# Optimization experiments

Measured on AMD Instinct MI355X. Metric: run time of the kernel, lower is better.

The kernel has to match this reference:

```python
import jax, jax.numpy as jnp
import numpy as np

WIN = (7, 7)          # window_size (M, M)
DIM = 128             # C
HEADS = 4
B = 64                # images
NW = 64               # windows per image
NG = WIN[0] * WIN[1]  # 49 tokens per window
NT = 3136             # total patches per image (56x56)


def _relative_position_index(wh, ww):
    # Faithful to the TF code (default 'xy' meshgrid ordering, global token at (0,0))
    coords = np.stack(np.meshgrid(np.arange(wh), np.arange(ww)))        # (2, ww, wh)
    flat = coords.reshape(2, wh * ww)                                    # (2, M^2)
    flat1 = np.concatenate([flat, np.array([[0], [0]])], axis=1)         # (2, M^2+1)
    rel = flat[:, :, None] - flat1[:, None, :]                           # (2, M^2, M^2+1)
    rel = rel.transpose(1, 2, 0).astype(np.int32)
    rel[:, :, 0] += wh - 1
    rel[:, :, 1] += ww - 1
    rel[:, :, 0] *= 2 * ww - 1
    return rel.sum(-1)                                                   # (M^2, M^2+1)


def setup_inputs() -> dict:
    key = jax.random.key(0)
    ks = jax.random.split(key, 9)
    C, H = DIM, HEADS
    B_ = B * NW
    table_sz = (2 * WIN[0] - 1) * (2 * WIN[1] - 1)  # 169
    return {
        "x": jax.random.normal(ks[0], (B_, NG, C), jnp.float32),
        "xtotal": jax.random.normal(ks[1], (B, NT, C), jnp.float32),
        "xavg": jax.random.normal(ks[2], (B, 1, C), jnp.float32),
        "mask": jnp.zeros((NW, NG, NG + 1), jnp.float32),
        "W_q": jax.random.normal(ks[3], (C, C), jnp.float32) * (C ** -0.5),
        "b_q": jax.random.normal(ks[4], (C,), jnp.float32) * 0.02,
        "W_kv": jax.random.normal(ks[5], (C, 2 * C), jnp.float32) * (C ** -0.5),
        "b_kv": jax.random.normal(ks[6], (2 * C,), jnp.float32) * 0.02,
        "bias_table": jax.random.normal(ks[7], (table_sz, H), jnp.float32) * 0.02,
        "rel_idx": jnp.asarray(_relative_position_index(*WIN), jnp.int32),
    }


def reference(x, xtotal, xavg, mask, W_q, b_q, W_kv, b_kv, bias_table, rel_idx):
    B_, NGl, C = x.shape
    Bl = xavg.shape[0]
    H = bias_table.shape[1]
    d = C // H
    scale = d ** -0.5
    N = NGl + 1

    # window path: concat repeated global token, project kv / q
    xavgR = jnp.repeat(xavg, B_ // Bl, axis=0)               # (B_, 1, C)
    x_c = jnp.concatenate([x, xavgR], axis=1)                # (B_, N, C)
    kv = (x_c @ W_kv + b_kv).reshape(B_, N, 2, H, d).transpose(2, 0, 3, 1, 4)
    k, v = kv[0], kv[1]                                      # (B_, H, N, d)
    q = ((x @ W_q + b_q).reshape(B_, NGl, H, d).transpose(0, 2, 1, 3)) * scale

    attn = jnp.einsum('bhnd,bhmd->bhnm', q, k)               # (B_, H, NG, N)
    bias = bias_table[rel_idx.reshape(-1)].reshape(NGl, N, H).transpose(2, 0, 1)
    attn = attn + bias[None]
    nW = mask.shape[0]
    attn = attn.reshape(B_ // nW, nW, H, NGl, N) + mask[None, :, None]
    attn = jax.nn.softmax(attn.reshape(B_, H, NGl, N), axis=-1)
    x_out = jnp.einsum('bhnm,bhmd->bhnd', attn, v).transpose(0, 2, 1, 3).reshape(B_, NGl, C)

    # global path: q_avg (NOT scaled in the original), attends over all patches
    Nt = xtotal.shape[1]
    kvg = (xtotal @ W_kv + b_kv).reshape(Bl, Nt, 2, H, d).transpose(2, 0, 3, 1, 4)
    kg, vg = kvg[0], kvg[1]                                  # (B, H, Nt, d)
    q_avg = (xavg @ W_q + b_q).reshape(Bl, 1, H, d).transpose(0, 2, 1, 3)
    attng = jax.nn.softmax(jnp.einsum('bhqd,bhmd->bhqm', q_avg, kg), axis=-1)
    xavg_out = jnp.einsum('bhqm,bhmd->bhqd', attng, vg).transpose(0, 2, 1, 3).reshape(Bl, 1, C)
    return x_out, xavg_out
```

## Files before the change

### kernel.cpp

```cpp
#include <hip/hip_runtime.h>
#include <hip/hip_bf16.h>

#define NB_  4096
#define NG_  49
#define NC_  128
#define NH_  4
#define DH_  32
#define NN_  50
#define NIMG 64
#define NT_  3136
#define NCHK 8
#define CROWS 392
#define SCALE_ 0.17677669529663687f

#define WT_LO_OFF 49152
#define BM_OFF    98304
#define FBASE  573440
#define U_F    (FBASE)
#define CST_F  (FBASE + 32768)
#define WACC_F (FBASE + 33024)
#define SUM_F  (FBASE + 65792)
#define CNT_F  (FBASE + 66048)

typedef unsigned short u16;
typedef unsigned int   u32;
typedef __attribute__((ext_vector_type(8))) short bf16x8;
typedef __attribute__((ext_vector_type(4))) float f32x4;

__device__ __forceinline__ float b2f(u16 u) {
    union { u32 i; float f; } v; v.i = ((u32)u) << 16; return v.f;
}
__device__ __forceinline__ u16 f2b(float f) {
    union { float f; u32 i; } v; v.f = f;
    u32 x = v.i;
    return (u16)((x + 0x7fffu + ((x >> 16) & 1u)) >> 16);
}
__device__ __forceinline__ u32 pk2(float a, float b) {
    union { __hip_bfloat162 h2; u32 u; } v;
    v.h2 = __float22bfloat162_rn(make_float2(a, b));
    return v.u;
}

extern "C" __global__ __launch_bounds__(256)
void prep_kernel(const float* __restrict__ Wq, const float* __restrict__ Wkv,
                 const float* __restrict__ btab, const int* __restrict__ ridx,
                 const float* __restrict__ mask, const float* __restrict__ xavg,
                 const float* __restrict__ bq, const float* __restrict__ bkv,
                 u16* __restrict__ ws)
{
    __shared__ int   ridxS[NG_ * NN_];
    __shared__ float btabS[169 * NH_];
    __shared__ float xavgS[NC_];
    __shared__ float qaS[NC_];
    const int t = threadIdx.x, b = blockIdx.x;
    if (b < 24) {
        const int fp  = b * 4 + (t >> 6);
        const int lane = t & 63, l15 = lane & 15, g = lane >> 4;
        const int kt = fp & 3, rest = fp >> 2, jt = rest & 1, hty = rest >> 1;
        const int ty = hty % 3, hh = hty / 3;
        const int jc = 32 * hh + 16 * jt + l15;
        const float* src; int stride; float qs = 1.f;
        if (ty == 0)      { src = Wq  + jc;       stride = NC_;     qs = SCALE_; }
        else if (ty == 1) { src = Wkv + jc;       stride = 2 * NC_; }
        else              { src = Wkv + NC_ + jc; stride = 2 * NC_; }
        const int c0 = 32 * kt + 8 * g;
        u32 hi[4], lo[4];
        #pragma unroll
        for (int p = 0; p < 4; ++p) {
            const int c = c0 + 2 * p;
            float w0 = src[(size_t)c * stride] * qs;
            float w1 = src[(size_t)(c + 1) * stride] * qs;
            u16 h0 = f2b(w0), h1 = f2b(w1);
            hi[p] = (u32)h0 | ((u32)h1 << 16);
            lo[p] = (u32)f2b(w0 - b2f(h0)) | ((u32)f2b(w1 - b2f(h1)) << 16);
        }
        const size_t fo = ((size_t)fp * 64 + lane) * 8;
        *(uint4*)(ws + fo)             = make_uint4(hi[0], hi[1], hi[2], hi[3]);
        *(uint4*)(ws + WT_LO_OFF + fo) = make_uint4(lo[0], lo[1], lo[2], lo[3]);
    } else if (b < 88) {
        const int wx = b - 24;
        for (int i = t; i < NG_ * NN_; i += 256) ridxS[i] = ridx[i];
        for (int i = t; i < 169 * NH_; i += 256) btabS[i] = btab[i];
        __syncthreads();
        for (int i = t; i < NH_ * 16 * 64; i += 256) {
            const int lane = i & 63, tile = (i >> 6) & 15, h = i >> 10;
            const int n  = 16 * (tile >> 2) + (lane & 15);
            const int m0 = 16 * (tile & 3) + 4 * (lane >> 4);
            u16 vv[4];
            #pragma unroll
            for (int e = 0; e < 4; ++e) {
                const int m = m0 + e;
                float val = -1e30f;
                if (n < NG_ && m < NN_)
                    val = btabS[ridxS[n * NN_ + m] * NH_ + h] + mask[((size_t)wx * NG_ + n) * NN_ + m];
                vv[e] = f2b(val);
            }
            u32* dst = (u32*)(ws + BM_OFF + ((size_t)((wx * NH_ + h) * 16 + tile) * 64 + lane) * 4);
            dst[0] = (u32)vv[0] | ((u32)vv[1] << 16);
            dst[1] = (u32)vv[2] | ((u32)vv[3] << 16);
        }
    } else {
        const int img = b - 88;
        float* wsF = (float*)ws;
        if (t < NC_) xavgS[t] = xavg[img * NC_ + t];
        __syncthreads();
        if (t < NC_) {
            float acc = bq[t];
            for (int c = 0; c < NC_; ++c) acc += xavgS[c] * Wq[c * NC_ + t];
            qaS[t] = acc;
        }
        __syncthreads();
        if (t < NC_) {
            const int c = t;
            const float* wr = Wkv + (size_t)c * 256;
            #pragma unroll
            for (int h = 0; h < NH_; ++h) {
                float acc = 0.f;
                #pragma unroll
                for (int j = 0; j < 32; ++j) acc += wr[h * 32 + j] * qaS[h * 32 + j];
                wsF[U_F + img * 512 + h * 128 + c] = acc;
            }
            #pragma unroll
            for (int h = 0; h < NH_; ++h) wsF[WACC_F + img * 512 + h * 128 + t] = 0.f;
        } else if (t < NC_ + NH_) {
            const int h = t - NC_;
            float acc = 0.f;
            for (int j = 0; j < 32; ++j) acc += qaS[h * 32 + j] * bkv[h * 32 + j];
            wsF[CST_F + img * 4 + h] = acc;
            wsF[SUM_F + img * 4 + h] = 0.f;
        } else if (t == NC_ + NH_) {
            ((int*)wsF)[CNT_F + img] = 0;
        }
    }
}

struct ChunkShared {
    float waccS[4][4][128];
    float esumS[4][4];
    float sumS[4];
    int   flagS;
};

extern "C" __global__ __launch_bounds__(256, 3)
void wa2_kernel(const float* __restrict__ x, const float* __restrict__ xtotal,
                const float* __restrict__ xavg,
                const float* __restrict__ Wq, const float* __restrict__ bq,
                const float* __restrict__ Wkv, const float* __restrict__ bkv,
                float* __restrict__ out, u16* __restrict__ ws)
{
    __shared__ ChunkShared smc;
    const int t = threadIdx.x;
    const int blk = blockIdx.x;
    const int lane = t & 63, wv = t >> 6;

    if (blk >= NIMG * NCHK) {
        const int wb   = blk - NIMG * NCHK;
        const int img  = wb >> 6;
        const int widx = wb & 63;
        const int h = wv, l15 = lane & 15, g = lane >> 4;

        bf16x8 xf[4][4];
        {
            const float* xbase = x + (size_t)wb * (NG_ * NC_);
            #pragma unroll
            for (int rt = 0; rt < 4; ++rt) {
                const int row = 16 * rt + l15;
                const float* rp = (row < NG_) ? (xbase + (size_t)row * NC_)
                                              : (xavg + (size_t)img * NC_);
                const bool vld = (row <= NG_);
                #pragma unroll
                for (int kt = 0; kt < 4; ++kt) {
                    float4 u0 = *(const float4*)(rp + 32 * kt + 8 * g);
                    float4 u1 = *(const float4*)(rp + 32 * kt + 8 * g + 4);
                    if (!vld) { u0 = make_float4(0.f,0.f,0.f,0.f); u1 = make_float4(0.f,0.f,0.f,0.f); }
                    union { u32 w[4]; bf16x8 v; } F;
                    F.w[0] = pk2(u0.x, u0.y); F.w[1] = pk2(u0.z, u0.w);
                    F.w[2] = pk2(u1.x, u1.y); F.w[3] = pk2(u1.z, u1.w);
                    xf[rt][kt] = F.v;
                }
            }
        }

        bf16x8 qf[4], kf[4];
        #pragma unroll
        for (int ty = 0; ty < 2; ++ty) {
            f32x4 acc[2][4];
            #pragma unroll
            for (int jt = 0; jt < 2; ++jt) {
                f32x4 cin;
                #pragma unroll
                for (int r = 0; r < 4; ++r) {
                    const int j = 32 * h + 16 * jt + 4 * g + r;
                    cin[r] = (ty == 0) ? bq[j] * SCALE_ : bkv[j];
                }
                #pragma unroll
                for (int rt = 0; rt < 4; ++rt) acc[jt][rt] = cin;
            }
            #pragma unroll
            for (int kt = 0; kt < 4; ++kt) {
                const int fpb = ((h * 3 + ty) * 2) * 4 + kt;
                const bf16x8 wh0 = *(const bf16x8*)(ws + ((size_t)fpb * 64 + lane) * 8);
                const bf16x8 wl0 = *(const bf16x8*)(ws + WT_LO_OFF + ((size_t)fpb * 64 + lane) * 8);
                const bf16x8 wh1 = *(const bf16x8*)(ws + ((size_t)(fpb + 4) * 64 + lane) * 8);
                const bf16x8 wl1 = *(const bf16x8*)(ws + WT_LO_OFF + ((size_t)(fpb + 4) * 64 + lane) * 8);
                #pragma unroll
                for (int rt = 0; rt < 4; ++rt) {
                    acc[0][rt] = __builtin_amdgcn_mfma_f32_16x16x32_bf16(wh0, xf[rt][kt], acc[0][rt], 0, 0, 0);
                    acc[0][rt] = __builtin_amdgcn_mfma_f32_16x16x32_bf16(wl0, xf[rt][kt], acc[0][rt], 0, 0, 0);
                    acc[1][rt] = __builtin_amdgcn_mfma_f32_16x16x32_bf16(wh1, xf[rt][kt], acc[1][rt], 0, 0, 0);
                    acc[1][rt] = __builtin_amdgcn_mfma_f32_16x16x32_bf16(wl1, xf[rt][kt], acc[1][rt], 0, 0, 0);
                }
            }
            #pragma unroll
            for (int rt = 0; rt < 4; ++rt) {
                union { u32 w[4]; bf16x8 v; } F;
                F.w[0] = pk2(acc[0][rt][0], acc[0][rt][1]);
                F.w[1] = pk2(acc[0][rt][2], acc[0][rt][3]);
                F.w[2] = pk2(acc[1][rt][0], acc[1][rt][1]);
                F.w[3] = pk2(acc[1][rt][2], acc[1][rt][3]);
                if (ty == 0) qf[rt] = F.v; else kf[rt] = F.v;
            }
        }

        bf16x8 vbf[2][2];
        {
            f32x4 vacc[4][2];
            #pragma unroll
            for (int tn = 0; tn < 2; ++tn) {
                const float bv = bkv[NC_ + 32 * h + 16 * tn + l15];
                #pragma unroll
                for (int tm = 0; tm < 4; ++tm) vacc[tm][tn] = (f32x4){bv, bv, bv, bv};
            }
            #pragma unroll
            for (int kt = 0; kt < 4; ++kt) {
                const int fpb = ((h * 3 + 2) * 2) * 4 + kt;
                const bf16x8 wh0 = *(const bf16x8*)(ws + ((size_t)fpb * 64 + lane) * 8);
                const bf16x8 wl0 = *(const bf16x8*)(ws + WT_LO_OFF + ((size_t)fpb * 64 + lane) * 8);
                const bf16x8 wh1 = *(const bf16x8*)(ws + ((size_t)(fpb + 4) * 64 + lane) * 8);
                const bf16x8 wl1 = *(const bf16x8*)(ws + WT_LO_OFF + ((size_t)(fpb + 4) * 64 + lane) * 8);
                #pragma unroll
                for (int tm = 0; tm < 4; ++tm) {
                    vacc[tm][0] = __builtin_amdgcn_mfma_f32_16x16x32_bf16(xf[tm][kt], wh0, vacc[tm][0], 0, 0, 0);
                    vacc[tm][0] = __builtin_amdgcn_mfma_f32_16x16x32_bf16(xf[tm][kt], wl0, vacc[tm][0], 0, 0, 0);
                    vacc[tm][1] = __builtin_amdgcn_mfma_f32_16x16x32_bf16(xf[tm][kt], wh1, vacc[tm][1], 0, 0, 0);
                    vacc[tm][1] = __builtin_amdgcn_mfma_f32_16x16x32_bf16(xf[tm][kt], wl1, vacc[tm][1], 0, 0, 0);
                }
            }
            #pragma unroll
            for (int kt2 = 0; kt2 < 2; ++kt2)
                #pragma unroll
                for (int tn = 0; tn < 2; ++tn) {
                    union { u32 w[4]; bf16x8 v; } F;
                    F.w[0] = pk2(vacc[2 * kt2][tn][0], vacc[2 * kt2][tn][1]);
                    F.w[1] = pk2(vacc[2 * kt2][tn][2], vacc[2 * kt2][tn][3]);
                    F.w[2] = pk2(vacc[2 * kt2 + 1][tn][0], vacc[2 * kt2 + 1][tn][1]);
                    F.w[3] = pk2(vacc[2 * kt2 + 1][tn][2], vacc[2 * kt2 + 1][tn][3]);
                    vbf[kt2][tn] = F.v;
                }
        }

        const u16* bmb = ws + BM_OFF + (size_t)(widx * NH_ + h) * 4096;
        #pragma unroll
        for (int tq = 0; tq < 4; ++tq) {
            f32x4 s[4];
            #pragma unroll
            for (int tk = 0; tk < 4; ++tk) {
                uint2 bm = *(const uint2*)(bmb + ((size_t)(tq * 4 + tk) * 64 + lane) * 4);
                f32x4 c0;
                c0[0] = b2f((u16)bm.x); c0[1] = b2f((u16)(bm.x >> 16));
                c0[2] = b2f((u16)bm.y); c0[3] = b2f((u16)(bm.y >> 16));
                s[tk] = __builtin_amdgcn_mfma_f32_16x16x32_bf16(kf[tk], qf[tq], c0, 0, 0, 0);
            }
            float mx = s[0][0];
            #pragma unroll
            for (int tk = 0; tk < 4; ++tk)
                #pragma unroll
                for (int r = 0; r < 4; ++r) mx = fmaxf(mx, s[tk][r]);
            mx = fmaxf(mx, __shfl_xor(mx, 16));
            mx = fmaxf(mx, __shfl_xor(mx, 32));
            float sum = 0.f;
            #pragma unroll
            for (int tk = 0; tk < 4; ++tk)
                #pragma unroll
                for (int r = 0; r < 4; ++r) {
                    float e = __expf(s[tk][r] - mx);
                    s[tk][r] = e;
                    sum += e;
                }
            sum += __shfl_xor(sum, 16);
            sum += __shfl_xor(sum, 32);
            const float inv = 1.f / sum;

            bf16x8 pa[2];
            #pragma unroll
            for (int kt2 = 0; kt2 < 2; ++kt2) {
                union { u32 w[4]; bf16x8 v; } P;
                P.w[0] = pk2(s[2 * kt2][0] * inv, s[2 * kt2][1] * inv);
                P.w[1] = pk2(s[2 * kt2][2] * inv, s[2 * kt2][3] * inv);
                P.w[2] = pk2(s[2 * kt2 + 1][0] * inv, s[2 * kt2 + 1][1] * inv);
                P.w[3] = pk2(s[2 * kt2 + 1][2] * inv, s[2 * kt2 + 1][3] * inv);
                pa[kt2] = P.v;
            }
            #pragma unroll
            for (int tn = 0; tn < 2; ++tn) {
                f32x4 o = {0.f, 0.f, 0.f, 0.f};
                o = __builtin_amdgcn_mfma_f32_16x16x32_bf16(pa[0], vbf[0][tn], o, 0, 0, 0);
                o = __builtin_amdgcn_mfma_f32_16x16x32_bf16(pa[1], vbf[1][tn], o, 0, 0, 0);
                #pragma unroll
                for (int r = 0; r < 4; ++r) {
                    const int row = 16 * tq + 4 * g + r;
                    if (row < NG_)
                        out[(size_t)wb * (NG_ * NC_) + (size_t)row * NC_ + 32 * h + 16 * tn + l15] = o[r];
                }
            }
        }
    } else {
        ChunkShared& S = smc;
        float* wsF = (float*)ws;
        const int img = blk >> 3, ch = blk & 7;
        const int c0 = (lane & 31) * 4, roff = lane >> 5;

        float4 uR[NH_]; float cstR[NH_];
        #pragma unroll
        for (int h = 0; h < NH_; ++h) {
            uR[h]  = *(const float4*)&wsF[U_F + img * 512 + h * 128 + c0];
            cstR[h] = wsF[CST_F + img * 4 + h];
        }

        float wacc[NH_][4] = {};
        float esum[NH_] = {0.f, 0.f, 0.f, 0.f};
        const float* xb = xtotal + ((size_t)img * NT_ + ch * CROWS) * NC_;
        for (int it = 0; it < CROWS / 8; ++it) {
            const int m = it * 8 + wv * 2 + roff;
            float4 xv = *(const float4*)&xb[(size_t)m * NC_ + c0];
            float s[NH_];
            #pragma unroll
            for (int h = 0; h < NH_; ++h)
                s[h] = xv.x * uR[h].x + xv.y * uR[h].y + xv.z * uR[h].z + xv.w * uR[h].w;
            #pragma unroll
            for (int off = 1; off < 32; off <<= 1) {
                #pragma unroll
                for (int h = 0; h < NH_; ++h) s[h] += __shfl_xor(s[h], off);
            }
            #pragma unroll
            for (int h = 0; h < NH_; ++h) {
                const float e = __expf(s[h] + cstR[h]);
                wacc[h][0] += e * xv.x; wacc[h][1] += e * xv.y;
                wacc[h][2] += e * xv.z; wacc[h][3] += e * xv.w;
                if ((lane & 31) == 0) esum[h] += e;
            }
        }

        #pragma unroll
        for (int h = 0; h < NH_; ++h) {
            #pragma unroll
            for (int i = 0; i < 4; ++i) wacc[h][i] += __shfl_xor(wacc[h][i], 32);
            esum[h] += __shfl_xor(esum[h], 32);
        }
        if (lane < 32) {
            #pragma unroll
            for (int h = 0; h < NH_; ++h)
                #pragma unroll
                for (int i = 0; i < 4; ++i) S.waccS[wv][h][c0 + i] = wacc[h][i];
            if (lane == 0) {
                #pragma unroll
                for (int h = 0; h < NH_; ++h) S.esumS[wv][h] = esum[h];
            }
        }
        __syncthreads();
        if (t < NC_) {
            #pragma unroll
            for (int h = 0; h < NH_; ++h) {
                float v = S.waccS[0][h][t] + S.waccS[1][h][t] + S.waccS[2][h][t] + S.waccS[3][h][t];
                atomicAdd(&wsF[WACC_F + img * 512 + h * 128 + t], v);
            }
        } else if (t < NC_ + NH_) {
            const int h = t - NC_;
            atomicAdd(&wsF[SUM_F + img * 4 + h],
                      S.esumS[0][h] + S.esumS[1][h] + S.esumS[2][h] + S.esumS[3][h]);
        }
        __threadfence();
        __syncthreads();
        if (t == 0) S.flagS = atomicAdd(&((int*)wsF)[CNT_F + img], 1);
        __syncthreads();
        if (S.flagS == NCHK - 1) {
            float* wS = &S.waccS[0][0][0];
            for (int i = t; i < 512; i += 256)
                wS[i] = atomicAdd(&wsF[WACC_F + img * 512 + i], 0.f);
            if (t < NH_) S.sumS[t] = atomicAdd(&wsF[SUM_F + img * 4 + t], 0.f);
            __syncthreads();
            if (t < NC_) {
                const int h = t >> 5;
                const float inv = 1.f / S.sumS[h];
                float acc = bkv[NC_ + t];
                for (int c = 0; c < NC_; ++c)
                    acc += (wS[h * 128 + c] * inv) * Wkv[(size_t)c * 256 + NC_ + t];
                out[(size_t)NB_ * (NG_ * NC_) + img * NC_ + t] = acc;
            }
        }
    }
}

extern "C" void kernel_launch(void* const* d_in, const int* in_sizes, int n_in,
                              void* d_out, int out_size, void* d_ws, size_t ws_size,
                              hipStream_t stream) {
    const float* x      = (const float*)d_in[0];
    const float* xtotal = (const float*)d_in[1];
    const float* xavg   = (const float*)d_in[2];
    const float* mask   = (const float*)d_in[3];
    const float* Wq     = (const float*)d_in[4];
    const float* bq     = (const float*)d_in[5];
    const float* Wkv    = (const float*)d_in[6];
    const float* bkv    = (const float*)d_in[7];
    const float* btab   = (const float*)d_in[8];
    const int*   ridx   = (const int*)d_in[9];
    float* outp = (float*)d_out;
    u16*   ws   = (u16*)d_ws;
    (void)in_sizes; (void)n_in; (void)out_size; (void)ws_size;

    prep_kernel<<<152, 256, 0, stream>>>(Wq, Wkv, btab, ridx, mask, xavg, bq, bkv, ws);
    wa2_kernel<<<NIMG * NCHK + NB_, 256, 0, stream>>>(x, xtotal, xavg, Wq, bq,
                                                      Wkv, bkv, outp, ws);
}
```

Baseline: 426.6 us.

## Stream x fragments per k-step, interleave weight hi/lo, raise occupancy, drop softmax max

Result: slower. 552.7 us (+29.6%).

```diff
diff --git a/kernel.cpp b/kernel.cpp
--- a/kernel.cpp
+++ b/kernel.cpp
@@ -13,7 +13,6 @@
 #define CROWS 392
 #define SCALE_ 0.17677669529663687f
 
-#define WT_LO_OFF 49152
 #define BM_OFF    98304
 #define FBASE  573440
 #define U_F    (FBASE)
@@ -39,6 +38,26 @@
     union { __hip_bfloat162 h2; u32 u; } v;
     v.h2 = __float22bfloat162_rn(make_float2(a, b));
     return v.u;
+}
+
+__device__ __forceinline__ void load_xf(const float* __restrict__ xbase,
+                                        const float* __restrict__ xavgp,
+                                        int kt, int l15, int g, bf16x8* xf)
+{
+    #pragma unroll
+    for (int rt = 0; rt < 4; ++rt) {
+        const int row = 16 * rt + l15;
+        const float* rp = (row < NG_) ? (xbase + (size_t)row * NC_) : xavgp;
+        const bool vld = (row <= NG_);
+        float4 u0 = *(const float4*)(rp + 32 * kt + 8 * g);
+        float4 u1 = *(const float4*)(rp + 32 * kt + 8 * g + 4);
+        union { u32 w[4]; bf16x8 v; } F;
+        F.w[0] = vld ? pk2(u0.x, u0.y) : 0u;
+        F.w[1] = vld ? pk2(u0.z, u0.w) : 0u;
+        F.w[2] = vld ? pk2(u1.x, u1.y) : 0u;
+        F.w[3] = vld ? pk2(u1.z, u1.w) : 0u;
+        xf[rt] = F.v;
+    }
 }
 
 extern "C" __global__ __launch_bounds__(256)
@@ -74,9 +93,9 @@
             hi[p] = (u32)h0 | ((u32)h1 << 16);
             lo[p] = (u32)f2b(w0 - b2f(h0)) | ((u32)f2b(w1 - b2f(h1)) << 16);
         }
-        const size_t fo = ((size_t)fp * 64 + lane) * 8;
-        *(uint4*)(ws + fo)             = make_uint4(hi[0], hi[1], hi[2], hi[3]);
-        *(uint4*)(ws + WT_LO_OFF + fo) = make_uint4(lo[0], lo[1], lo[2], lo[3]);
+        const size_t fo = ((size_t)fp * 64 + lane) * 16;
+        *(uint4*)(ws + fo)     = make_uint4(hi[0], hi[1], hi[2], hi[3]);
+        *(uint4*)(ws + fo + 8) = make_uint4(lo[0], lo[1], lo[2], lo[3]);
     } else if (b < 88) {
         const int wx = b - 24;
         for (int i = t; i < NG_ * NN_; i += 256) ridxS[i] = ridx[i];
@@ -141,7 +160,7 @@
     int   flagS;
 };
 
-extern "C" __global__ __launch_bounds__(256, 3)
+extern "C" __global__ __launch_bounds__(256, 4)
 void wa2_kernel(const float* __restrict__ x, const float* __restrict__ xtotal,
                 const float* __restrict__ xavg,
                 const float* __restrict__ Wq, const float* __restrict__ bq,
@@ -158,92 +177,89 @@
         const int img  = wb >> 6;
         const int widx = wb & 63;
         const int h = wv, l15 = lane & 15, g = lane >> 4;
-
-        bf16x8 xf[4][4];
+        const float* xbase = x + (size_t)wb * (NG_ * NC_);
+        const float* xavgp = xavg + (size_t)img * NC_;
+
+        bf16x8 qf[4], kf[4];
         {
-            const float* xbase = x + (size_t)wb * (NG_ * NC_);
-            #pragma unroll
-            for (int rt = 0; rt < 4; ++rt) {
-                const int row = 16 * rt + l15;
-                const float* rp = (row < NG_) ? (xbase + (size_t)row * NC_)
-                                              : (xavg + (size_t)img * NC_);
-                const bool vld = (row <= NG_);
-                #pragma unroll
-                for (int kt = 0; kt < 4; ++kt) {
-                    float4 u0 = *(const float4*)(rp + 32 * kt + 8 * g);
-                    float4 u1 = *(const float4*)(rp + 32 * kt + 8 * g + 4);
-                    if (!vld) { u0 = make_float4(0.f,0.f,0.f,0.f); u1 = make_float4(0.f,0.f,0.f,0.f); }
-                    union { u32 w[4]; bf16x8 v; } F;
-                    F.w[0] = pk2(u0.x, u0.y); F.w[1] = pk2(u0.z, u0.w);
-                    F.w[2] = pk2(u1.x, u1.y); F.w[3] = pk2(u1.z, u1.w);
-                    xf[rt][kt] = F.v;
-                }
-            }
-        }
-
-        bf16x8 qf[4], kf[4];
-        #pragma unroll
-        for (int ty = 0; ty < 2; ++ty) {
-            f32x4 acc[2][4];
+            f32x4 aq[2][4], ak[2][4];
             #pragma unroll
             for (int jt = 0; jt < 2; ++jt) {
-                f32x4 cin;
+                f32x4 cq, ck;
                 #pragma unroll
                 for (int r = 0; r < 4; ++r) {
                     const int j = 32 * h + 16 * jt + 4 * g + r;
-                    cin[r] = (ty == 0) ? bq[j] * SCALE_ : bkv[j];
-                }
-                #pragma unroll
-                for (int rt = 0; rt < 4; ++rt) acc[jt][rt] = cin;
+                    cq[r] = bq[j] * SCALE_;
+                    ck[r] = bkv[j];
+                }
+                #pragma unroll
+                for (int rt = 0; rt < 4; ++rt) { aq[jt][rt] = cq; ak[jt][rt] = ck; }
             }
             #pragma unroll
             for (int kt = 0; kt < 4; ++kt) {
-                const int fpb = ((h * 3 + ty) * 2) * 4 + kt;
-                const bf16x8 wh0 = *(const bf16x8*)(ws + ((size_t)fpb * 64 + lane) * 8);
-                const bf16x8 wl0 = *(const bf16x8*)(ws + WT_LO_OFF + ((size_t)fpb * 64 + lane) * 8);
-                const bf16x8 wh1 = *(const bf16x8*)(ws + ((size_t)(fpb + 4) * 64 + lane) * 8);
-                const bf16x8 wl1 = *(const bf16x8*)(ws + WT_LO_OFF + ((size_t)(fpb + 4) * 64 + lane) * 8);
+                bf16x8 xf[4];
+                load_xf(xbase, xavgp, kt, l15, g, xf);
+                const u16* wq0 = ws + ((size_t)((h * 3 + 0) * 8 + kt) * 64 + lane) * 16;
+                const u16* wk0 = ws + ((size_t)((h * 3 + 1) * 8 + kt) * 64 + lane) * 16;
+                const bf16x8 qh0 = *(const bf16x8*)(wq0);
+                const bf16x8 ql0 = *(const bf16x8*)(wq0 + 8);
+                const bf16x8 qh1 = *(const bf16x8*)(wq0 + 64 * 64);
+                const bf16x8 ql1 = *(const bf16x8*)(wq0 + 64 * 64 + 8);
+                const bf16x8 kh0 = *(const bf16x8*)(wk0);
+                const bf16x8 kl0 = *(const bf16x8*)(wk0 + 8);
+                const bf16x8 kh1 = *(const bf16x8*)(wk0 + 64 * 64);
+                const bf16x8 kl1 = *(const bf16x8*)(wk0 + 64 * 64 + 8);
                 #pragma unroll
                 for (int rt = 0; rt < 4; ++rt) {
-                    acc[0][rt] = __builtin_amdgcn_mfma_f32_16x16x32_bf16(wh0, xf[rt][kt], acc[0][rt], 0, 0, 0);
-                    acc[0][rt] = __builtin_amdgcn_mfma_f32_16x16x32_bf16(wl0, xf[rt][kt], acc[0][rt], 0, 0, 0);
-                    acc[1][rt] = __builtin_amdgcn_mfma_f32_16x16x32_bf16(wh1, xf[rt][kt], acc[1][rt], 0, 0, 0);
-                    acc[1][rt] = __builtin_amdgcn_mfma_f32_16x16x32_bf16(wl1, xf[rt][kt], acc[1][rt], 0, 0, 0);
+                    aq[0][rt] = __builtin_amdgcn_mfma_f32_16x16x32_bf16(qh0, xf[rt], aq[0][rt], 0, 0, 0);
+                    aq[0][rt] = __builtin_amdgcn_mfma_f32_16x16x32_bf16(ql0, xf[rt], aq[0][rt], 0, 0, 0);
+                    aq[1][rt] = __builtin_amdgcn_mfma_f32_16x16x32_bf16(qh1, xf[rt], aq[1][rt], 0, 0, 0);
+                    aq[1][rt] = __builtin_amdgcn_mfma_f32_16x16x32_bf16(ql1, xf[rt], aq[1][rt], 0, 0, 0);
+                    ak[0][rt] = __builtin_amdgcn_mfma_f32_16x16x32_bf16(kh0, xf[rt], ak[0][rt], 0, 0, 0);
+                    ak[0][rt] = __builtin_amdgcn_mfma_f32_16x16x32_bf16(kl0, xf[rt], ak[0][rt], 0, 0, 0);
+                    ak[1][rt] = __builtin_amdgcn_mfma_f32_16x16x32_bf16(kh1, xf[rt], ak[1][rt], 0, 0, 0);
+                    ak[1][rt] = __builtin_amdgcn_mfma_f32_16x16x32_bf16(kl1, xf[rt], ak[1][rt], 0, 0, 0);
                 }
             }
             #pragma unroll
             for (int rt = 0; rt < 4; ++rt) {
-                union { u32 w[4]; bf16x8 v; } F;
-                F.w[0] = pk2(acc[0][rt][0], acc[0][rt][1]);
-                F.w[1] = pk2(acc[0][rt][2], acc[0][rt][3]);
-                F.w[2] = pk2(acc[1][rt][0], acc[1][rt][1]);
-                F.w[3] = pk2(acc[1][rt][2], acc[1][rt][3]);
-                if (ty == 0) qf[rt] = F.v; else kf[rt] = F.v;
+                union { u32 w[4]; bf16x8 v; } FQ, FK;
+                FQ.w[0] = pk2(aq[0][rt][0], aq[0][rt][1]);
+                FQ.w[1] = pk2(aq[0][rt][2], aq[0][rt][3]);
+                FQ.w[2] = pk2(aq[1][rt][0], aq[1][rt][1]);
+                FQ.w[3] = pk2(aq[1][rt][2], aq[1][rt][3]);
+                FK.w[0] = pk2(ak[0][rt][0], ak[0][rt][1]);
+                FK.w[1] = pk2(ak[0][rt][2], ak[0][rt][3]);
+                FK.w[2] = pk2(ak[1][rt][0], ak[1][rt][1]);
+                FK.w[3] = pk2(ak[1][rt][2], ak[1][rt][3]);
+                qf[rt] = FQ.v; kf[rt] = FK.v;
             }
         }
 
         bf16x8 vbf[2][2];
         {
-            f32x4 vacc[4][2];
+            f32x4 av[4][2];
             #pragma unroll
             for (int tn = 0; tn < 2; ++tn) {
                 const float bv = bkv[NC_ + 32 * h + 16 * tn + l15];
                 #pragma unroll
-                for (int tm = 0; tm < 4; ++tm) vacc[tm][tn] = (f32x4){bv, bv, bv, bv};
+                for (int tm = 0; tm < 4; ++tm) av[tm][tn] = (f32x4){bv, bv, bv, bv};
             }
             #pragma unroll
             for (int kt = 0; kt < 4; ++kt) {
-                const int fpb = ((h * 3 + 2) * 2) * 4 + kt;
-                const bf16x8 wh0 = *(const bf16x8*)(ws + ((size_t)fpb * 64 + lane) * 8);
-                const bf16x8 wl0 = *(const bf16x8*)(ws + WT_LO_OFF + ((size_t)fpb * 64 + lane) * 8);
-                const bf16x8 wh1 = *(const bf16x8*)(ws + ((size_t)(fpb + 4) * 64 + lane) * 8);
-                const bf16x8 wl1 = *(const bf16x8*)(ws + WT_LO_OFF + ((size_t)(fpb + 4) * 64 + lane) * 8);
+                bf16x8 xf[4];
+                load_xf(xbase, xavgp, kt, l15, g, xf);
+                const u16* wv0 = ws + ((size_t)((h * 3 + 2) * 8 + kt) * 64 + lane) * 16;
+                const bf16x8 vh0 = *(const bf16x8*)(wv0);
+                const bf16x8 vl0 = *(const bf16x8*)(wv0 + 8);
+                const bf16x8 vh1 = *(const bf16x8*)(wv0 + 64 * 64);
+                const bf16x8 vl1 = *(const bf16x8*)(wv0 + 64 * 64 + 8);
                 #pragma unroll
                 for (int tm = 0; tm < 4; ++tm) {
-                    vacc[tm][0] = __builtin_amdgcn_mfma_f32_16x16x32_bf16(xf[tm][kt], wh0, vacc[tm][0], 0, 0, 0);
-                    vacc[tm][0] = __builtin_amdgcn_mfma_f32_16x16x32_bf16(xf[tm][kt], wl0, vacc[tm][0], 0, 0, 0);
-                    vacc[tm][1] = __builtin_amdgcn_mfma_f32_16x16x32_bf16(xf[tm][kt], wh1, vacc[tm][1], 0, 0, 0);
-                    vacc[tm][1] = __builtin_amdgcn_mfma_f32_16x16x32_bf16(xf[tm][kt], wl1, vacc[tm][1], 0, 0, 0);
+                    av[tm][0] = __builtin_amdgcn_mfma_f32_16x16x32_bf16(xf[tm], vh0, av[tm][0], 0, 0, 0);
+                    av[tm][0] = __builtin_amdgcn_mfma_f32_16x16x32_bf16(xf[tm], vl0, av[tm][0], 0, 0, 0);
+                    av[tm][1] = __builtin_amdgcn_mfma_f32_16x16x32_bf16(xf[tm], vh1, av[tm][1], 0, 0, 0);
+                    av[tm][1] = __builtin_amdgcn_mfma_f32_16x16x32_bf16(xf[tm], vl1, av[tm][1], 0, 0, 0);
                 }
             }
             #pragma unroll
@@ -251,10 +267,10 @@
                 #pragma unroll
                 for (int tn = 0; tn < 2; ++tn) {
                     union { u32 w[4]; bf16x8 v; } F;
-                    F.w[0] = pk2(vacc[2 * kt2][tn][0], vacc[2 * kt2][tn][1]);
-                    F.w[1] = pk2(vacc[2 * kt2][tn][2], vacc[2 * kt2][tn][3]);
-                    F.w[2] = pk2(vacc[2 * kt2 + 1][tn][0], vacc[2 * kt2 + 1][tn][1]);
-                    F.w[3] = pk2(vacc[2 * kt2 + 1][tn][2], vacc[2 * kt2 + 1][tn][3]);
+                    F.w[0] = pk2(av[2 * kt2][tn][0], av[2 * kt2][tn][1]);
+                    F.w[1] = pk2(av[2 * kt2][tn][2], av[2 * kt2][tn][3]);
+                    F.w[2] = pk2(av[2 * kt2 + 1][tn][0], av[2 * kt2 + 1][tn][1]);
+                    F.w[3] = pk2(av[2 * kt2 + 1][tn][2], av[2 * kt2 + 1][tn][3]);
                     vbf[kt2][tn] = F.v;
                 }
         }
@@ -271,19 +287,12 @@
                 c0[2] = b2f((u16)bm.y); c0[3] = b2f((u16)(bm.y >> 16));
                 s[tk] = __builtin_amdgcn_mfma_f32_16x16x32_bf16(kf[tk], qf[tq], c0, 0, 0, 0);
             }
-            float mx = s[0][0];
+            float sum = 0.f;
             #pragma unroll
             for (int tk = 0; tk < 4; ++tk)
                 #pragma unroll
-                for (int r = 0; r < 4; ++r) mx = fmaxf(mx, s[tk][r]);
-            mx = fmaxf(mx, __shfl_xor(mx, 16));
-            mx = fmaxf(mx, __shfl_xor(mx, 32));
-            float sum = 0.f;
-            #pragma unroll
-            for (int tk = 0; tk < 4; ++tk)
-                #pragma unroll
                 for (int r = 0; r < 4; ++r) {
-                    float e = __expf(s[tk][r] - mx);
+                    float e = __expf(s[tk][r]);
                     s[tk][r] = e;
                     sum += e;
                 }
```
